# Performance work log

Hardware: AMD Instinct MI355X
Metric: run time of the kernel (lower is better)

The kernel has to match this reference:

```python
import jax, jax.numpy as jnp
import numpy as np
from jax import lax

B, C, H, W = 8, 64, 256, 256
LENGTH = 9
REDUCTION = 8
HIDDEN = max(8, C // REDUCTION)


def _conv(x, w, b, pad):
    # x: [B,Cin,H,W], w: [Cout,Cin,kh,kw]
    y = lax.conv_general_dilated(x, w, (1, 1), [(pad, pad), (pad, pad)],
                                 dimension_numbers=('NCHW', 'OIHW', 'NCHW'))
    return y + b[None, :, None, None]


def _bilinear(img, cy, cx):
    # img: [B,C,H,W]; cy,cx: [B,H,W] float coords already clipped to [0, size-1]
    # Matches F.grid_sample(mode='bilinear', padding_mode='border', align_corners=True)
    Hh, Ww = img.shape[2], img.shape[3]
    y0 = jnp.floor(cy)
    x0 = jnp.floor(cx)
    wy = (cy - y0)[:, None]  # [B,1,H,W]
    wx = (cx - x0)[:, None]
    y0i = y0.astype(jnp.int32)
    x0i = x0.astype(jnp.int32)
    y1i = jnp.minimum(y0i + 1, Hh - 1)
    x1i = jnp.minimum(x0i + 1, Ww - 1)

    def g(im, iy, ix):
        return im[:, iy, ix]  # [C,H,W]

    gather = jax.vmap(g)
    v00 = gather(img, y0i, x0i)
    v01 = gather(img, y0i, x1i)
    v10 = gather(img, y1i, x0i)
    v11 = gather(img, y1i, x1i)
    return (v00 * (1 - wy) * (1 - wx) + v01 * (1 - wy) * wx
            + v10 * wy * (1 - wx) + v11 * wy * wx)


def _oriented_pool(x, vx, vy, length):
    # x: [B,C,H,W]; vx,vy: [B,1,H,W] direction fields
    _, _, Hh, Ww = x.shape
    yy = jnp.arange(Hh, dtype=x.dtype)[None, :, None]  # [1,H,1]
    xx = jnp.arange(Ww, dtype=x.dtype)[None, None, :]  # [1,1,W]
    half = length // 2
    offsets = jnp.arange(-half, half + 1, dtype=x.dtype)
    vx2 = vx[:, 0]  # [B,H,W]
    vy2 = vy[:, 0]

    def step(acc, t):
        cy = jnp.clip(yy + t * vy2, 0.0, Hh - 1)
        cx = jnp.clip(xx + t * vx2, 0.0, Ww - 1)
        return acc + _bilinear(x, cy, cx), None

    acc, _ = lax.scan(step, jnp.zeros_like(x), offsets)
    return acc / length


def setup_inputs() -> dict:
    key = jax.random.key(0)
    ks = jax.random.split(key, 5)

    def he(k, shape, fan_in):
        return jax.random.normal(k, shape, jnp.float32) * np.float32(1.0 / np.sqrt(fan_in))

    return {
        'x': jax.random.normal(ks[0], (B, C, H, W), jnp.float32),
        'w3': he(ks[1], (HIDDEN, C, 3, 3), C * 9),
        'b3': jnp.zeros((HIDDEN,), jnp.float32),
        'w1': he(ks[2], (1, HIDDEN, 1, 1), HIDDEN),
        'b1': jnp.zeros((1,), jnp.float32),
        'wr': he(ks[3], (HIDDEN, 2 * C, 1, 1), 2 * C),
        'br': jnp.zeros((HIDDEN,), jnp.float32),
        'we': he(ks[4], (2 * C, HIDDEN, 1, 1), HIDDEN),
        'be': jnp.zeros((2 * C,), jnp.float32),
    }


def reference(x, w3, b3, w1, b1, wr, br, we, be):
    theta = jnp.pi * jax.nn.sigmoid(_conv(jax.nn.relu(_conv(x, w3, b3, 1)), w1, b1, 0))  # [B,1,H,W]
    cos_t = jnp.cos(theta)
    sin_t = jnp.sin(theta)
    tan_feat = _oriented_pool(x, cos_t, sin_t, LENGTH)
    nor_feat = _oriented_pool(x, -sin_t, cos_t, LENGTH)
    context = jnp.concatenate([tan_feat, nor_feat], axis=1)  # [B,2C,H,W]
    w = jax.nn.sigmoid(_conv(jax.nn.relu(_conv(context, wr, br, 0)), we, be, 0))  # [B,2C,H,W]
    alpha_tan, alpha_norm = jnp.split(w, 2, axis=1)
    return (alpha_tan + alpha_norm) * x
```

## Files before the change

### kernel.cpp

```cpp
#include <hip/hip_runtime.h>
#include <math.h>

#define Bb 8
#define Cc 64
#define Hh 256
#define Ww 256
#define HID 8
#define PLANE (Hh*Ww)

typedef float fvec4 __attribute__((ext_vector_type(4)));

#define T2H 6
#define T2W 66
#define T2P 67
#define T2N (T2H*T2W)

__global__ __launch_bounds__(256, 4) void theta_kernel(
    const float* __restrict__ x, const float* __restrict__ w3,
    const float* __restrict__ b3, const float* __restrict__ w1,
    const float* __restrict__ b1, float* __restrict__ cosout,
    float* __restrict__ sinout)
{
    __shared__ fvec4 tileA[T2H * T2P];
    __shared__ fvec4 tileB[T2H * T2P];
    const int tid = threadIdx.x;
    const int tx = tid & 63;
    const int ty = tid >> 6;
    const int xx = blockIdx.x * 64 + tx;
    const int yy = blockIdx.y * 4 + ty;
    const int b  = blockIdx.z;
    const int row0 = blockIdx.y * 4 - 1;
    const int col0 = blockIdx.x * 64 - 1;

    const float* xb = x + (size_t)b * Cc * PLANE;

    int goff[2], loff[2];
    bool intile[2], inimg[2];
    #pragma unroll
    for (int k = 0; k < 2; k++) {
        const int i  = tid + k * 256;
        const int r  = i / T2W;
        const int cc = i - r * T2W;
        const int gy = row0 + r;
        const int gx = col0 + cc;
        intile[k] = (i < T2N);
        inimg[k]  = intile[k] && gy >= 0 && gy < Hh && gx >= 0 && gx < Ww;
        goff[k] = inimg[k] ? (gy * Ww + gx) : 0;
        loff[k] = r * T2P + cc;
    }

    float acc[HID];
    #pragma unroll
    for (int h = 0; h < HID; h++) acc[h] = 0.f;

    float rv[2][8];
    #pragma unroll
    for (int k = 0; k < 2; k++)
        #pragma unroll
        for (int q = 0; q < 8; q++) rv[k][q] = 0.f;
    #pragma unroll
    for (int k = 0; k < 2; k++) if (inimg[k]) {
        #pragma unroll
        for (int q = 0; q < 8; q++) rv[k][q] = xb[goff[k] + (size_t)q * PLANE];
    }

    const int lbase = (ty + 1) * T2P + (tx + 1);

    for (int st = 0; st < Cc / 8; st++) {
        __syncthreads();
        #pragma unroll
        for (int k = 0; k < 2; k++) if (intile[k]) {
            tileA[loff[k]] = (fvec4){rv[k][0], rv[k][1], rv[k][2], rv[k][3]};
            tileB[loff[k]] = (fvec4){rv[k][4], rv[k][5], rv[k][6], rv[k][7]};
        }
        if (st + 1 < Cc / 8) {
            const float* xn = xb + (size_t)(st + 1) * 8 * PLANE;
            #pragma unroll
            for (int k = 0; k < 2; k++) if (inimg[k]) {
                #pragma unroll
                for (int q = 0; q < 8; q++)
                    rv[k][q] = xn[goff[k] + (size_t)q * PLANE];
            }
        }
        __syncthreads();

        fvec4 va[9], vb[9];
        #pragma unroll
        for (int dy = 0; dy < 3; dy++)
            #pragma unroll
            for (int dx = 0; dx < 3; dx++) {
                va[dy * 3 + dx] = tileA[lbase + (dy - 1) * T2P + (dx - 1)];
                vb[dy * 3 + dx] = tileB[lbase + (dy - 1) * T2P + (dx - 1)];
            }

        #pragma unroll
        for (int h = 0; h < HID; h++) {
            const float* wk = w3 + (size_t)(h * Cc + st * 8) * 9;
            float a = acc[h];
            #pragma unroll
            for (int c = 0; c < 4; c++)
                #pragma unroll
                for (int k = 0; k < 9; k++)
                    a = fmaf(wk[c * 9 + k], va[k][c], a);
            #pragma unroll
            for (int c = 0; c < 4; c++)
                #pragma unroll
                for (int k = 0; k < 9; k++)
                    a = fmaf(wk[(4 + c) * 9 + k], vb[k][c], a);
            acc[h] = a;
        }
    }

    float z = b1[0];
    #pragma unroll
    for (int h = 0; h < HID; h++) {
        float hr = acc[h] + b3[h];
        hr = hr > 0.f ? hr : 0.f;
        z = fmaf(w1[h], hr, z);
    }
    const float theta = 3.14159265358979f / (1.f + __expf(-z));
    float s, co;
    __sincosf(theta, &s, &co);
    const int p = b * PLANE + yy * Ww + xx;
    cosout[p] = co;
    sinout[p] = s;
}

#define TPH 13
#define TPW 74
#define TPP 75
#define TPN (TPH*TPW)

__global__ __launch_bounds__(256, 3) void pool_kernel(
    const float* __restrict__ x,
    const float* __restrict__ cosb, const float* __restrict__ sinb,
    const float* __restrict__ wr, const float* __restrict__ br,
    const float* __restrict__ we, const float* __restrict__ be,
    float* __restrict__ out)
{
    __shared__ fvec4 tile[TPH * TPP];
    const int tid = threadIdx.x;
    const int tx = tid & 63;
    const int ty = tid >> 6;
    const int xx = blockIdx.x * 64 + tx;
    const int yy = blockIdx.y * 4 + ty;
    const int b  = blockIdx.z;
    const int p  = b * PLANE + yy * Ww + xx;
    const int row0 = blockIdx.y * 4 - 4;
    const int col0 = blockIdx.x * 64 - 4;

    const float vx = cosb[p];
    const float vy = sinb[p];

    int   off[16];
    float fwy[16], fwx[16];
    #pragma unroll
    for (int s = 0; s < 9; s++) {
        if (s == 4) continue;
        const int j = (s < 4) ? s : s - 1;
        const float t = (float)(s - 4);
        float cy = fminf(fmaxf((float)yy + t * vy, 0.f), (float)(Hh - 1));
        float cx = fminf(fmaxf((float)xx + t * vx, 0.f), (float)(Ww - 1));
        int y0 = min((int)cy, Hh - 2);
        int x0 = min((int)cx, Ww - 2);
        off[j] = (y0 - row0) * TPP + (x0 - col0);
        fwy[j] = cy - (float)y0;
        fwx[j] = cx - (float)x0;
        float cy2 = fminf(fmaxf((float)yy + t * vx, 0.f), (float)(Hh - 1));
        float cx2 = fminf(fmaxf((float)xx - t * vy, 0.f), (float)(Ww - 1));
        int y02 = min((int)cy2, Hh - 2);
        int x02 = min((int)cx2, Ww - 2);
        off[8 + j] = (y02 - row0) * TPP + (x02 - col0);
        fwy[8 + j] = cy2 - (float)y02;
        fwx[8 + j] = cx2 - (float)x02;
    }
    #pragma unroll
    for (int s = 0; s < 16; s++)
        asm volatile("" : "+v"(off[s]), "+v"(fwx[s]), "+v"(fwy[s]));

    const int lcen = (ty + 4) * TPP + (tx + 4);

    int goff[4], loff[4];
    #pragma unroll
    for (int k = 0; k < 4; k++) {
        int i = tid + k * 256;
        i = (i < TPN) ? i : (TPN - 1);
        const int r  = i / TPW;
        const int cc = i - r * TPW;
        const int gy = min(max(row0 + r, 0), Hh - 1);
        const int gx = min(max(col0 + cc, 0), Ww - 1);
        goff[k] = gy * Ww + gx;
        loff[k] = r * TPP + cc;
    }
    #pragma unroll
    for (int k = 0; k < 4; k++)
        asm volatile("" : "+v"(goff[k]), "+v"(loff[k]));

    float hid[HID];
    #pragma unroll
    for (int h = 0; h < HID; h++) hid[h] = br[h];

    const float* xb = x + (size_t)b * Cc * PLANE;

    float rv[4][4];
    #pragma unroll
    for (int k = 0; k < 4; k++)
        #pragma unroll
        for (int q = 0; q < 4; q++)
            rv[k][q] = xb[goff[k] + (size_t)q * PLANE];

    for (int cp = 0; cp < Cc / 4; cp++) {
        __syncthreads();
        #pragma unroll
        for (int k = 0; k < 4; k++)
            tile[loff[k]] = (fvec4){rv[k][0], rv[k][1], rv[k][2], rv[k][3]};
        if (cp + 1 < Cc / 4) {
            const float* xn = xb + (size_t)(cp + 1) * 4 * PLANE;
            #pragma unroll
            for (int k = 0; k < 4; k++)
                #pragma unroll
                for (int q = 0; q < 4; q++)
                    rv[k][q] = xn[goff[k] + (size_t)q * PLANE];
        }
        __syncthreads();

        const fvec4 cent = tile[lcen];
        float tac[4], nac[4];
        #pragma unroll
        for (int q = 0; q < 4; q++) { tac[q] = cent[q]; nac[q] = cent[q]; }

        #pragma unroll
        for (int s = 0; s < 16; s++) {
            const int o = off[s];
            const fvec4 a00 = tile[o];
            const fvec4 a01 = tile[o + 1];
            const fvec4 a10 = tile[o + TPP];
            const fvec4 a11 = tile[o + TPP + 1];
            const float wx_ = fwx[s], wy_ = fwy[s];
            #pragma unroll
            for (int q = 0; q < 4; q++) {
                const float tq = a00[q] + wx_ * (a01[q] - a00[q]);
                const float bq = a10[q] + wx_ * (a11[q] - a10[q]);
                const float vq = tq + wy_ * (bq - tq);
                if (s < 8) tac[q] += vq; else nac[q] += vq;
            }
        }
        const int c = 4 * cp;
        #pragma unroll
        for (int q = 0; q < 4; q++) {
            const float tq = tac[q] * (1.f / 9.f);
            const float nq = nac[q] * (1.f / 9.f);
            #pragma unroll
            for (int h = 0; h < HID; h++) {
                float a = hid[h];
                a = fmaf(wr[h * 128 + c + q],      tq, a);
                a = fmaf(wr[h * 128 + 64 + c + q], nq, a);
                hid[h] = a;
            }
        }
    }

    #pragma unroll
    for (int h = 0; h < HID; h++) hid[h] = fmaxf(hid[h], 0.f);

    const int pix = yy * Ww + xx;
    for (int c = 0; c < Cc; c++) {
        float z1 = be[c];
        float z2 = be[c + 64];
        #pragma unroll
        for (int h = 0; h < HID; h++) {
            z1 = fmaf(we[c * 8 + h],        hid[h], z1);
            z2 = fmaf(we[(c + 64) * 8 + h], hid[h], z2);
        }
        const float a1 = 1.f / (1.f + __expf(-z1));
        const float a2 = 1.f / (1.f + __expf(-z2));
        const float xv = xb[c * PLANE + pix];
        out[(size_t)(b * Cc + c) * PLANE + pix] = (a1 + a2) * xv;
    }
}

extern "C" void kernel_launch(void* const* d_in, const int* in_sizes, int n_in,
                              void* d_out, int out_size, void* d_ws, size_t ws_size,
                              hipStream_t stream) {
    const float* x  = (const float*)d_in[0];
    const float* w3 = (const float*)d_in[1];
    const float* b3 = (const float*)d_in[2];
    const float* w1 = (const float*)d_in[3];
    const float* b1 = (const float*)d_in[4];
    const float* wr = (const float*)d_in[5];
    const float* br = (const float*)d_in[6];
    const float* we = (const float*)d_in[7];
    const float* be = (const float*)d_in[8];
    float* out = (float*)d_out;

    float* cosb = (float*)d_ws;
    float* sinb = cosb + (size_t)Bb * PLANE;

    dim3 grid(Ww / 64, Hh / 4, Bb);
    dim3 block(256);
    theta_kernel<<<grid, block, 0, stream>>>(x, w3, b3, w1, b1, cosb, sinb);
    pool_kernel<<<grid, block, 0, stream>>>(x, cosb, sinb, wr, br, we, be, out);
}
```

Baseline: 530.6 us.

## Fuse theta conv into pooling kernel and precompute bilinear corner weights

Merges the 3x3-conv theta computation into the pooling kernel. The kernel reuses the pooling tile (4-channel slabs with a 4-pixel halo) for the conv, so cos/sin no longer go through global memory and one launch is removed. The conv pass masks out-of-image taps only on border blocks. The last prefetch wraps to channel 0 so the pooling pass can start with its data already loaded. Bilinear interpolation now uses four precomputed corner weights with FMAs instead of lerps. In exchange, x is streamed through shared memory twice per block and register pressure rises from the extra weight arrays.

```diff
diff --git a/kernel.cpp b/kernel.cpp
--- a/kernel.cpp
+++ b/kernel.cpp
@@ -10,130 +10,15 @@
 
 typedef float fvec4 __attribute__((ext_vector_type(4)));
 
-#define T2H 6
-#define T2W 66
-#define T2P 67
-#define T2N (T2H*T2W)
-
-__global__ __launch_bounds__(256, 4) void theta_kernel(
-    const float* __restrict__ x, const float* __restrict__ w3,
-    const float* __restrict__ b3, const float* __restrict__ w1,
-    const float* __restrict__ b1, float* __restrict__ cosout,
-    float* __restrict__ sinout)
-{
-    __shared__ fvec4 tileA[T2H * T2P];
-    __shared__ fvec4 tileB[T2H * T2P];
-    const int tid = threadIdx.x;
-    const int tx = tid & 63;
-    const int ty = tid >> 6;
-    const int xx = blockIdx.x * 64 + tx;
-    const int yy = blockIdx.y * 4 + ty;
-    const int b  = blockIdx.z;
-    const int row0 = blockIdx.y * 4 - 1;
-    const int col0 = blockIdx.x * 64 - 1;
-
-    const float* xb = x + (size_t)b * Cc * PLANE;
-
-    int goff[2], loff[2];
-    bool intile[2], inimg[2];
-    #pragma unroll
-    for (int k = 0; k < 2; k++) {
-        const int i  = tid + k * 256;
-        const int r  = i / T2W;
-        const int cc = i - r * T2W;
-        const int gy = row0 + r;
-        const int gx = col0 + cc;
-        intile[k] = (i < T2N);
-        inimg[k]  = intile[k] && gy >= 0 && gy < Hh && gx >= 0 && gx < Ww;
-        goff[k] = inimg[k] ? (gy * Ww + gx) : 0;
-        loff[k] = r * T2P + cc;
-    }
-
-    float acc[HID];
-    #pragma unroll
-    for (int h = 0; h < HID; h++) acc[h] = 0.f;
-
-    float rv[2][8];
-    #pragma unroll
-    for (int k = 0; k < 2; k++)
-        #pragma unroll
-        for (int q = 0; q < 8; q++) rv[k][q] = 0.f;
-    #pragma unroll
-    for (int k = 0; k < 2; k++) if (inimg[k]) {
-        #pragma unroll
-        for (int q = 0; q < 8; q++) rv[k][q] = xb[goff[k] + (size_t)q * PLANE];
-    }
-
-    const int lbase = (ty + 1) * T2P + (tx + 1);
-
-    for (int st = 0; st < Cc / 8; st++) {
-        __syncthreads();
-        #pragma unroll
-        for (int k = 0; k < 2; k++) if (intile[k]) {
-            tileA[loff[k]] = (fvec4){rv[k][0], rv[k][1], rv[k][2], rv[k][3]};
-            tileB[loff[k]] = (fvec4){rv[k][4], rv[k][5], rv[k][6], rv[k][7]};
-        }
-        if (st + 1 < Cc / 8) {
-            const float* xn = xb + (size_t)(st + 1) * 8 * PLANE;
-            #pragma unroll
-            for (int k = 0; k < 2; k++) if (inimg[k]) {
-                #pragma unroll
-                for (int q = 0; q < 8; q++)
-                    rv[k][q] = xn[goff[k] + (size_t)q * PLANE];
-            }
-        }
-        __syncthreads();
-
-        fvec4 va[9], vb[9];
-        #pragma unroll
-        for (int dy = 0; dy < 3; dy++)
-            #pragma unroll
-            for (int dx = 0; dx < 3; dx++) {
-                va[dy * 3 + dx] = tileA[lbase + (dy - 1) * T2P + (dx - 1)];
-                vb[dy * 3 + dx] = tileB[lbase + (dy - 1) * T2P + (dx - 1)];
-            }
-
-        #pragma unroll
-        for (int h = 0; h < HID; h++) {
-            const float* wk = w3 + (size_t)(h * Cc + st * 8) * 9;
-            float a = acc[h];
-            #pragma unroll
-            for (int c = 0; c < 4; c++)
-                #pragma unroll
-                for (int k = 0; k < 9; k++)
-                    a = fmaf(wk[c * 9 + k], va[k][c], a);
-            #pragma unroll
-            for (int c = 0; c < 4; c++)
-                #pragma unroll
-                for (int k = 0; k < 9; k++)
-                    a = fmaf(wk[(4 + c) * 9 + k], vb[k][c], a);
-            acc[h] = a;
-        }
-    }
-
-    float z = b1[0];
-    #pragma unroll
-    for (int h = 0; h < HID; h++) {
-        float hr = acc[h] + b3[h];
-        hr = hr > 0.f ? hr : 0.f;
-        z = fmaf(w1[h], hr, z);
-    }
-    const float theta = 3.14159265358979f / (1.f + __expf(-z));
-    float s, co;
-    __sincosf(theta, &s, &co);
-    const int p = b * PLANE + yy * Ww + xx;
-    cosout[p] = co;
-    sinout[p] = s;
-}
-
 #define TPH 13
 #define TPW 74
 #define TPP 75
 #define TPN (TPH*TPW)
 
-__global__ __launch_bounds__(256, 3) void pool_kernel(
+__global__ __launch_bounds__(256, 3) void fused_kernel(
     const float* __restrict__ x,
-    const float* __restrict__ cosb, const float* __restrict__ sinb,
+    const float* __restrict__ w3, const float* __restrict__ b3,
+    const float* __restrict__ w1, const float* __restrict__ b1,
     const float* __restrict__ wr, const float* __restrict__ br,
     const float* __restrict__ we, const float* __restrict__ be,
     float* __restrict__ out)
@@ -145,40 +30,8 @@
     const int xx = blockIdx.x * 64 + tx;
     const int yy = blockIdx.y * 4 + ty;
     const int b  = blockIdx.z;
-    const int p  = b * PLANE + yy * Ww + xx;
     const int row0 = blockIdx.y * 4 - 4;
     const int col0 = blockIdx.x * 64 - 4;
-
-    const float vx = cosb[p];
-    const float vy = sinb[p];
-
-    int   off[16];
-    float fwy[16], fwx[16];
-    #pragma unroll
-    for (int s = 0; s < 9; s++) {
-        if (s == 4) continue;
-        const int j = (s < 4) ? s : s - 1;
-        const float t = (float)(s - 4);
-        float cy = fminf(fmaxf((float)yy + t * vy, 0.f), (float)(Hh - 1));
-        float cx = fminf(fmaxf((float)xx + t * vx, 0.f), (float)(Ww - 1));
-        int y0 = min((int)cy, Hh - 2);
-        int x0 = min((int)cx, Ww - 2);
-        off[j] = (y0 - row0) * TPP + (x0 - col0);
-        fwy[j] = cy - (float)y0;
-        fwx[j] = cx - (float)x0;
-        float cy2 = fminf(fmaxf((float)yy + t * vx, 0.f), (float)(Hh - 1));
-        float cx2 = fminf(fmaxf((float)xx - t * vy, 0.f), (float)(Ww - 1));
-        int y02 = min((int)cy2, Hh - 2);
-        int x02 = min((int)cx2, Ww - 2);
-        off[8 + j] = (y02 - row0) * TPP + (x02 - col0);
-        fwy[8 + j] = cy2 - (float)y02;
-        fwx[8 + j] = cx2 - (float)x02;
-    }
-    #pragma unroll
-    for (int s = 0; s < 16; s++)
-        asm volatile("" : "+v"(off[s]), "+v"(fwx[s]), "+v"(fwy[s]));
-
-    const int lcen = (ty + 4) * TPP + (tx + 4);
 
     int goff[4], loff[4];
     #pragma unroll
@@ -196,11 +49,19 @@
     for (int k = 0; k < 4; k++)
         asm volatile("" : "+v"(goff[k]), "+v"(loff[k]));
 
-    float hid[HID];
-    #pragma unroll
-    for (int h = 0; h < HID; h++) hid[h] = br[h];
-
+    const int lcen = (ty + 4) * TPP + (tx + 4);
     const float* xb = x + (size_t)b * Cc * PLANE;
+
+    const bool interior = (blockIdx.y > 0) && (blockIdx.y < (Hh/4 - 1)) &&
+                          (blockIdx.x > 0) && (blockIdx.x < (Ww/64 - 1));
+    float mk[9];
+    #pragma unroll
+    for (int dy = 0; dy < 3; dy++)
+        #pragma unroll
+        for (int dx = 0; dx < 3; dx++) {
+            const int gy = yy + dy - 1, gx = xx + dx - 1;
+            mk[dy*3+dx] = (gy >= 0 && gy < Hh && gx >= 0 && gx < Ww) ? 1.f : 0.f;
+        }
 
     float rv[4][4];
     #pragma unroll
@@ -208,6 +69,102 @@
         #pragma unroll
         for (int q = 0; q < 4; q++)
             rv[k][q] = xb[goff[k] + (size_t)q * PLANE];
+
+    float acc[HID];
+    #pragma unroll
+    for (int h = 0; h < HID; h++) acc[h] = 0.f;
+
+    for (int st = 0; st < Cc / 4; st++) {
+        __syncthreads();
+        #pragma unroll
+        for (int k = 0; k < 4; k++)
+            tile[loff[k]] = (fvec4){rv[k][0], rv[k][1], rv[k][2], rv[k][3]};
+        {
+            const int nst = (st + 1 < Cc / 4) ? st + 1 : 0;
+            const float* xn = xb + (size_t)nst * 4 * PLANE;
+            #pragma unroll
+            for (int k = 0; k < 4; k++)
+                #pragma unroll
+                for (int q = 0; q < 4; q++)
+                    rv[k][q] = xn[goff[k] + (size_t)q * PLANE];
+        }
+        __syncthreads();
+
+        fvec4 va[9];
+        #pragma unroll
+        for (int dy = 0; dy < 3; dy++)
+            #pragma unroll
+            for (int dx = 0; dx < 3; dx++)
+                va[dy*3+dx] = tile[lcen + (dy - 1) * TPP + (dx - 1)];
+        if (!interior) {
+            #pragma unroll
+            for (int k = 0; k < 9; k++) va[k] *= mk[k];
+        }
+        #pragma unroll
+        for (int h = 0; h < HID; h++) {
+            const float* wk = w3 + (size_t)(h * Cc + st * 4) * 9;
+            float a = acc[h];
+            #pragma unroll
+            for (int q = 0; q < 4; q++)
+                #pragma unroll
+                for (int k = 0; k < 9; k++)
+                    a = fmaf(wk[q * 9 + k], va[k][q], a);
+            acc[h] = a;
+        }
+    }
+
+    float z = b1[0];
+    #pragma unroll
+    for (int h = 0; h < HID; h++) {
+        float hr = acc[h] + b3[h];
+        hr = hr > 0.f ? hr : 0.f;
+        z = fmaf(w1[h], hr, z);
+    }
+    const float theta = 3.14159265358979f / (1.f + __expf(-z));
+    float vy, vx;
+    __sincosf(theta, &vy, &vx);
+
+    int   off[16];
+    float cw00[16], cw01[16], cw10[16], cw11[16];
+    #pragma unroll
+    for (int s = 0; s < 9; s++) {
+        if (s == 4) continue;
+        const int j = (s < 4) ? s : s - 1;
+        const float t = (float)(s - 4);
+        {
+            float cy = fminf(fmaxf((float)yy + t * vy, 0.f), (float)(Hh - 1));
+            float cx = fminf(fmaxf((float)xx + t * vx, 0.f), (float)(Ww - 1));
+            int y0 = min((int)cy, Hh - 2);
+            int x0 = min((int)cx, Ww - 2);
+            off[j] = (y0 - row0) * TPP + (x0 - col0);
+            const float wy = cy - (float)y0, wx = cx - (float)x0;
+            cw00[j] = (1.f - wy) * (1.f - wx);
+            cw01[j] = (1.f - wy) * wx;
+            cw10[j] = wy * (1.f - wx);
+            cw11[j] = wy * wx;
+        }
+        {
+            float cy = fminf(fmaxf((float)yy + t * vx, 0.f), (float)(Hh - 1));
+            float cx = fminf(fmaxf((float)xx - t * vy, 0.f), (float)(Ww - 1));
+            int y0 = min((int)cy, Hh - 2);
+            int x0 = min((int)cx, Ww - 2);
+            off[8 + j] = (y0 - row0) * TPP + (x0 - col0);
+            const float wy = cy - (float)y0, wx = cx - (float)x0;
+            cw00[8 + j] = (1.f - wy) * (1.f - wx);
+            cw01[8 + j] = (1.f - wy) * wx;
+            cw10[8 + j] = wy * (1.f - wx);
+            cw11[8 + j] = wy * wx;
+        }
+    }
+    #pragma unroll
+    for (int s = 0; s < 16; s++) {
+        asm volatile("" : "+v"(off[s]), "+v"(cw00[s]), "+v"(cw01[s]));
+        asm volatile("" : "+v"(cw10[s]), "+v"(cw11[s]));
+    }
+
+    float hid[HID];
+    #pragma unroll
+    for (int h = 0; h < HID; h++) hid[h] = br[h];
 
     for (int cp = 0; cp < Cc / 4; cp++) {
         __syncthreads();
@@ -236,13 +193,16 @@
             const fvec4 a01 = tile[o + 1];
             const fvec4 a10 = tile[o + TPP];
             const fvec4 a11 = tile[o + TPP + 1];
-            const float wx_ = fwx[s], wy_ = fwy[s];
+            const float u00 = cw00[s], u01 = cw01[s];
+            const float u10 = cw10[s], u11 = cw11[s];
             #pragma unroll
             for (int q = 0; q < 4; q++) {
-                const float tq = a00[q] + wx_ * (a01[q] - a00[q]);
-                const float bq = a10[q] + wx_ * (a11[q] - a10[q]);
-                const float vq = tq + wy_ * (bq - tq);
-                if (s < 8) tac[q] += vq; else nac[q] += vq;
+                float a = (s < 8) ? tac[q] : nac[q];
+                a = fmaf(a00[q], u00, a);
+                a = fmaf(a01[q], u01, a);
+                a = fmaf(a10[q], u10, a);
+                a = fmaf(a11[q], u11, a);
+                if (s < 8) tac[q] = a; else nac[q] = a;
             }
         }
         const int c = 4 * cp;
@@ -293,11 +253,8 @@
     const float* be = (const float*)d_in[8];
     float* out = (float*)d_out;
 
-    float* cosb = (float*)d_ws;
-    float* sinb = cosb + (size_t)Bb * PLANE;
-
     dim3 grid(Ww / 64, Hh / 4, Bb);
     dim3 block(256);
-    theta_kernel<<<grid, block, 0, stream>>>(x, w3, b3, w1, b1, cosb, sinb);
-    pool_kernel<<<grid, block, 0, stream>>>(x, cosb, sinb, wr, br, we, be, out);
+    fused_kernel<<<grid, block, 0, stream>>>(x, w3, b3, w1, b1,
+                                             wr, br, we, be, out);
 }
```

Measured after the change: 527.8 us. No clear change (-0.5%).
